# Kernel tuning notes

Measured on AMD Instinct MI355X. Metric: run time of the kernel, lower is better.

## Reference

```python
import jax, jax.numpy as jnp
import numpy as np


def _gcn_conv(x, W, b, src, dst, deg_inv_sqrt, n_nodes):
    # x: [N, Fin], W: [Fin, Fout]; edges (with self-loops): src, dst [E+N]
    h = x @ W  # [N, Fout]
    norm = deg_inv_sqrt[src] * deg_inv_sqrt[dst]  # [E+N]
    msgs = h[src] * norm[:, None]  # gather-multiply
    out = jax.ops.segment_sum(msgs, dst, num_segments=n_nodes)  # scatter-add
    return out + b


def setup_inputs() -> dict:
    key = jax.random.key(0)
    k1, k2, k3, k4 = jax.random.split(key, 4)
    N, E, FIN, HID, OUT = 100000, 3200000, 128, 32, 32
    x = jax.random.normal(k1, (N, FIN), dtype=jnp.float32)
    edge_index = jax.random.randint(k2, (2, E), 0, N, dtype=jnp.int64)
    W1 = jax.random.normal(k3, (FIN, HID), dtype=jnp.float32) * (1.0 / np.sqrt(FIN))
    b1 = jnp.zeros((HID,), dtype=jnp.float32)
    W2 = jax.random.normal(k4, (HID, OUT), dtype=jnp.float32) * (1.0 / np.sqrt(HID))
    b2 = jnp.zeros((OUT,), dtype=jnp.float32)
    return {"x": x, "edge_index": edge_index, "W1": W1, "b1": b1, "W2": W2, "b2": b2}


def reference(x, edge_index, W1, b1, W2, b2):
    n = x.shape[0]
    # GCNConv defaults: add self-loops, symmetric normalization D^-1/2 (A+I) D^-1/2
    loops = jnp.arange(n, dtype=edge_index.dtype)
    src = jnp.concatenate([edge_index[0], loops])
    dst = jnp.concatenate([edge_index[1], loops])
    deg = jax.ops.segment_sum(jnp.ones_like(dst, dtype=x.dtype), dst, num_segments=n)
    deg_inv_sqrt = jnp.where(deg > 0, jax.lax.rsqrt(jnp.maximum(deg, 1.0)), 0.0)
    h = jax.nn.relu(_gcn_conv(x, W1, b1, src, dst, deg_inv_sqrt, n))  # hidden layer + ReLU
    out = jax.nn.relu(_gcn_conv(h, W2, b2, src, dst, deg_inv_sqrt, n))  # last layer + last_activation relu
    return out
```

## Files before the change

kernel.cpp:

```cpp
#include <hip/hip_runtime.h>
#include <hip/hip_fp16.h>

#define FIN 128
#define HID 32
#define BSHIFT 8
#define BNODES 256
#define CHUNK 2048
#define NBMAX 512
#define CAPB 8960
#define G1ROWS 64
#define XPAD 4


__global__ __launch_bounds__(256) void chunk_sort_kernel(const int* __restrict__ src,
                                                         const int* __restrict__ dst,
                                                         int* __restrict__ ec,
                                                         unsigned short* __restrict__ offt,
                                                         int E, int nb) {
    __shared__ int hist[NBMAX];
    __shared__ int pref[NBMAX];
    __shared__ int wsum[128];
    __shared__ int sorted[CHUNK];
    int c = blockIdx.x, t = threadIdx.x;
    int beg = c * CHUNK;
    int cnt = min(CHUNK, E - beg);
    for (int i = t; i < nb; i += 256) hist[i] = 0;
    __syncthreads();
    int bk[8], ent[8];
    #pragma unroll
    for (int j = 0; j < 8; ++j) {
        int i = t + j * 256;
        if (i < cnt) {
            int d = dst[beg + i];
            bk[j]  = ((unsigned)d) >> BSHIFT;
            ent[j] = src[beg + i] | ((d & (BNODES - 1)) << 24);
            atomicAdd(&hist[bk[j]], 1);
        } else bk[j] = -1;
    }
    __syncthreads();
    if (t < 128) {
        int s = 0;
        #pragma unroll
        for (int j = 0; j < 4; ++j) {
            int idx = t * 4 + j;
            int v = (idx < nb) ? hist[idx] : 0;
            pref[idx] = s; s += v;
        }
        wsum[t] = s;
    }
    __syncthreads();
    if (t == 0) { int run = 0; for (int j = 0; j < 128; ++j) { int v = wsum[j]; wsum[j] = run; run += v; } }
    __syncthreads();
    for (int i = t; i < nb; i += 256) { int p = pref[i] + wsum[i >> 2]; pref[i] = p; hist[i] = p; }
    __syncthreads();
    #pragma unroll
    for (int j = 0; j < 8; ++j) {
        if (bk[j] >= 0) {
            int p = atomicAdd(&hist[bk[j]], 1);
            sorted[p] = ent[j];
        }
    }
    __syncthreads();
    for (int i = t; i < cnt; i += 256) ec[(size_t)c * CHUNK + i] = sorted[i];
    unsigned short* row = offt + (size_t)c * (nb + 1);
    for (int i = t; i < nb; i += 256) row[i] = (unsigned short)pref[i];
    if (t == 0) row[nb] = (unsigned short)cnt;
}


__global__ __launch_bounds__(1024) void bucket_build_kernel(const int* __restrict__ ec,
                                                            const unsigned short* __restrict__ offt,
                                                            int* __restrict__ entries,
                                                            float* __restrict__ dinv,
                                                            int* __restrict__ rowbeg,
                                                            int* __restrict__ rowcnt,
                                                            int n, int nb, int nchunks, int cap) {
    __shared__ int raw[CAPB];
    __shared__ int srt[CAPB];
    __shared__ int hist[BNODES];
    __shared__ int pref[BNODES];
    __shared__ int cursor[BNODES];
    __shared__ int wsum[64];
    __shared__ int nfill;
    int b = blockIdx.x, t = threadIdx.x;
    if (t < BNODES) hist[t] = 0;
    if (t == 0) nfill = 0;
    __syncthreads();
    for (int c = t; c < nchunks; c += 1024) {
        const unsigned short* row = offt + (size_t)c * (nb + 1);
        int s = row[b], e2 = row[b + 1];
        int m = e2 - s;
        if (m > 0) {
            int base = atomicAdd(&nfill, m);
            const int* p = ec + (size_t)c * CHUNK + s;
            for (int k = 0; k < m; ++k) {
                int e = p[k];
                if (base + k < CAPB) raw[base + k] = e;
                atomicAdd(&hist[((unsigned)e) >> 24], 1);
            }
        }
    }
    __syncthreads();
    int total = min(nfill, CAPB);
    if (t < 64) {
        int s = 0;
        #pragma unroll
        for (int j = 0; j < 4; ++j) { int v = hist[t * 4 + j]; pref[t * 4 + j] = s; s += v; }
        wsum[t] = s;
    }
    __syncthreads();
    if (t == 0) { int run = 0; for (int j = 0; j < 64; ++j) { int v = wsum[j]; wsum[j] = run; run += v; } }
    __syncthreads();
    if (t < BNODES) { int p = pref[t] + wsum[t >> 2]; pref[t] = p; cursor[t] = p; }
    __syncthreads();
    for (int i = t; i < total; i += 1024) {
        int e = raw[i];
        int p = atomicAdd(&cursor[((unsigned)e) >> 24], 1);
        srt[p] = e;
    }
    __syncthreads();
    int* ep = entries + (size_t)b * cap;
    for (int i = t; i < total; i += 1024) ep[i] = srt[i];
    int node = b * BNODES + t;
    if (t < BNODES && node < n) {
        int deg = hist[t];
        dinv[node]   = rsqrtf((float)deg + 1.0f);
        rowbeg[node] = b * cap + pref[t];
        rowcnt[node] = deg;
    }
}


__global__ __launch_bounds__(256) void gemm1_kernel(const float* __restrict__ x,
                                                    const float* __restrict__ W,
                                                    const float* __restrict__ dinv,
                                                    __half* __restrict__ h16, int n) {
    __shared__ float Ws[FIN * HID];
    __shared__ float xs[G1ROWS][FIN + XPAD];
    int t = threadIdx.x;
    for (int i = t; i < FIN * HID; i += 256) Ws[i] = W[i];
    int row0 = blockIdx.x * G1ROWS;
    for (int idx = t; idx < G1ROWS * (FIN / 4); idx += 256) {
        int r  = idx >> 5;
        int c4 = (idx & 31) * 4;
        int row = row0 + r;
        float4 v = (row < n) ? *(const float4*)&x[(size_t)row * FIN + c4]
                             : make_float4(0.f, 0.f, 0.f, 0.f);
        *(float4*)&xs[r][c4] = v;
    }
    __syncthreads();
    int tr = t >> 3, tc = t & 7;
    int r0 = tr * 2, c0 = tc * 4;
    float4 a0 = make_float4(0.f, 0.f, 0.f, 0.f);
    float4 a1 = make_float4(0.f, 0.f, 0.f, 0.f);
    #pragma unroll 8
    for (int k4 = 0; k4 < FIN / 4; ++k4) {
        float4 xv0 = *(const float4*)&xs[r0][k4 * 4];
        float4 xv1 = *(const float4*)&xs[r0 + 1][k4 * 4];
        float4 w0 = *(const float4*)&Ws[(k4 * 4 + 0) * HID + c0];
        float4 w1 = *(const float4*)&Ws[(k4 * 4 + 1) * HID + c0];
        float4 w2 = *(const float4*)&Ws[(k4 * 4 + 2) * HID + c0];
        float4 w3 = *(const float4*)&Ws[(k4 * 4 + 3) * HID + c0];
        a0.x = fmaf(xv0.x, w0.x, a0.x); a0.y = fmaf(xv0.x, w0.y, a0.y);
        a0.z = fmaf(xv0.x, w0.z, a0.z); a0.w = fmaf(xv0.x, w0.w, a0.w);
        a0.x = fmaf(xv0.y, w1.x, a0.x); a0.y = fmaf(xv0.y, w1.y, a0.y);
        a0.z = fmaf(xv0.y, w1.z, a0.z); a0.w = fmaf(xv0.y, w1.w, a0.w);
        a0.x = fmaf(xv0.z, w2.x, a0.x); a0.y = fmaf(xv0.z, w2.y, a0.y);
        a0.z = fmaf(xv0.z, w2.z, a0.z); a0.w = fmaf(xv0.z, w2.w, a0.w);
        a0.x = fmaf(xv0.w, w3.x, a0.x); a0.y = fmaf(xv0.w, w3.y, a0.y);
        a0.z = fmaf(xv0.w, w3.z, a0.z); a0.w = fmaf(xv0.w, w3.w, a0.w);
        a1.x = fmaf(xv1.x, w0.x, a1.x); a1.y = fmaf(xv1.x, w0.y, a1.y);
        a1.z = fmaf(xv1.x, w0.z, a1.z); a1.w = fmaf(xv1.x, w0.w, a1.w);
        a1.x = fmaf(xv1.y, w1.x, a1.x); a1.y = fmaf(xv1.y, w1.y, a1.y);
        a1.z = fmaf(xv1.y, w1.z, a1.z); a1.w = fmaf(xv1.y, w1.w, a1.w);
        a1.x = fmaf(xv1.z, w2.x, a1.x); a1.y = fmaf(xv1.z, w2.y, a1.y);
        a1.z = fmaf(xv1.z, w2.z, a1.z); a1.w = fmaf(xv1.z, w2.w, a1.w);
        a1.x = fmaf(xv1.w, w3.x, a1.x); a1.y = fmaf(xv1.w, w3.y, a1.y);
        a1.z = fmaf(xv1.w, w3.z, a1.z); a1.w = fmaf(xv1.w, w3.w, a1.w);
    }
    #pragma unroll
    for (int rr = 0; rr < 2; ++rr) {
        int row = row0 + r0 + rr;
        float4 a = rr ? a1 : a0;
        float sc = (row < n) ? dinv[row] : 0.f;
        __half2 p0 = __floats2half2_rn(a.x * sc, a.y * sc);
        __half2 p1 = __floats2half2_rn(a.z * sc, a.w * sc);
        __half2* dst = (__half2*)&h16[(size_t)row * HID + c0];
        dst[0] = p0;
        dst[1] = p1;
    }
}


__global__ __launch_bounds__(256) void gather_kernel(const int* __restrict__ entries,
                                                     const int* __restrict__ rowbeg,
                                                     const int* __restrict__ rowcnt,
                                                     const float* __restrict__ dinv,
                                                     const __half* __restrict__ h16,
                                                     const float* __restrict__ bias,
                                                     float* __restrict__ out, int n, int sent) {
    int t = threadIdx.x;
    int g = t >> 2, q = t & 3;
    int i = blockIdx.x * 64 + g;
    if (i >= n) return;
    float di = dinv[i];
    float s0, s1, s2, s3, s4, s5, s6, s7;
    {
        float4 raw = *(const float4*)&h16[(size_t)i * HID + q * 8];
        __half2 h0 = *(__half2*)&raw.x, h1 = *(__half2*)&raw.y;
        __half2 h2 = *(__half2*)&raw.z, h3 = *(__half2*)&raw.w;
        float2 f0 = __half22float2(h0), f1 = __half22float2(h1);
        float2 f2 = __half22float2(h2), f3 = __half22float2(h3);
        s0 = f0.x; s1 = f0.y; s2 = f1.x; s3 = f1.y;
        s4 = f2.x; s5 = f2.y; s6 = f3.x; s7 = f3.y;
    }
    int beg = rowbeg[i], cnt = rowcnt[i];
    for (int base = 0; base < cnt; base += 4) {
        int e[4];
        #pragma unroll
        for (int u = 0; u < 4; ++u)
            e[u] = (base + u < cnt) ? (entries[beg + base + u] & 0xFFFFFF) : sent;
        float4 raw[4];
        #pragma unroll
        for (int u = 0; u < 4; ++u)
            raw[u] = *(const float4*)&h16[(size_t)e[u] * HID + q * 8];
        #pragma unroll
        for (int u = 0; u < 4; ++u) {
            __half2 h0 = *(__half2*)&raw[u].x, h1 = *(__half2*)&raw[u].y;
            __half2 h2 = *(__half2*)&raw[u].z, h3 = *(__half2*)&raw[u].w;
            float2 f0 = __half22float2(h0), f1 = __half22float2(h1);
            float2 f2 = __half22float2(h2), f3 = __half22float2(h3);
            s0 += f0.x; s1 += f0.y; s2 += f1.x; s3 += f1.y;
            s4 += f2.x; s5 += f2.y; s6 += f3.x; s7 += f3.y;
        }
    }
    float4 b0 = *(const float4*)&bias[q * 8];
    float4 b1 = *(const float4*)&bias[q * 8 + 4];
    float4 o0, o1;
    o0.x = fmaxf(b0.x + di * s0, 0.f); o0.y = fmaxf(b0.y + di * s1, 0.f);
    o0.z = fmaxf(b0.z + di * s2, 0.f); o0.w = fmaxf(b0.w + di * s3, 0.f);
    o1.x = fmaxf(b1.x + di * s4, 0.f); o1.y = fmaxf(b1.y + di * s5, 0.f);
    o1.z = fmaxf(b1.z + di * s6, 0.f); o1.w = fmaxf(b1.w + di * s7, 0.f);
    float* op = &out[(size_t)i * HID + q * 8];
    *(float4*)op = o0;
    *(float4*)(op + 4) = o1;
}


__global__ __launch_bounds__(256) void gemm2_kernel(const float* __restrict__ hin,
                                                    const float* __restrict__ W,
                                                    const float* __restrict__ dinv,
                                                    __half* __restrict__ h16, int n) {
    __shared__ float Ws[HID * HID];
    __shared__ float hs[G1ROWS][HID + XPAD];
    int t = threadIdx.x;
    for (int i = t; i < HID * HID; i += 256) Ws[i] = W[i];
    int row0 = blockIdx.x * G1ROWS;
    for (int idx = t; idx < G1ROWS * (HID / 4); idx += 256) {
        int r  = idx >> 3;
        int c4 = (idx & 7) * 4;
        int row = row0 + r;
        float4 v = (row < n) ? *(const float4*)&hin[(size_t)row * HID + c4]
                             : make_float4(0.f, 0.f, 0.f, 0.f);
        *(float4*)&hs[r][c4] = v;
    }
    __syncthreads();
    int tr = t >> 3, tc = t & 7;
    int r0 = tr * 2, c0 = tc * 4;
    float4 a0 = make_float4(0.f, 0.f, 0.f, 0.f);
    float4 a1 = make_float4(0.f, 0.f, 0.f, 0.f);
    #pragma unroll
    for (int k4 = 0; k4 < HID / 4; ++k4) {
        float4 xv0 = *(const float4*)&hs[r0][k4 * 4];
        float4 xv1 = *(const float4*)&hs[r0 + 1][k4 * 4];
        float4 w0 = *(const float4*)&Ws[(k4 * 4 + 0) * HID + c0];
        float4 w1 = *(const float4*)&Ws[(k4 * 4 + 1) * HID + c0];
        float4 w2 = *(const float4*)&Ws[(k4 * 4 + 2) * HID + c0];
        float4 w3 = *(const float4*)&Ws[(k4 * 4 + 3) * HID + c0];
        a0.x = fmaf(xv0.x, w0.x, a0.x); a0.y = fmaf(xv0.x, w0.y, a0.y);
        a0.z = fmaf(xv0.x, w0.z, a0.z); a0.w = fmaf(xv0.x, w0.w, a0.w);
        a0.x = fmaf(xv0.y, w1.x, a0.x); a0.y = fmaf(xv0.y, w1.y, a0.y);
        a0.z = fmaf(xv0.y, w1.z, a0.z); a0.w = fmaf(xv0.y, w1.w, a0.w);
        a0.x = fmaf(xv0.z, w2.x, a0.x); a0.y = fmaf(xv0.z, w2.y, a0.y);
        a0.z = fmaf(xv0.z, w2.z, a0.z); a0.w = fmaf(xv0.z, w2.w, a0.w);
        a0.x = fmaf(xv0.w, w3.x, a0.x); a0.y = fmaf(xv0.w, w3.y, a0.y);
        a0.z = fmaf(xv0.w, w3.z, a0.z); a0.w = fmaf(xv0.w, w3.w, a0.w);
        a1.x = fmaf(xv1.x, w0.x, a1.x); a1.y = fmaf(xv1.x, w0.y, a1.y);
        a1.z = fmaf(xv1.x, w0.z, a1.z); a1.w = fmaf(xv1.x, w0.w, a1.w);
        a1.x = fmaf(xv1.y, w1.x, a1.x); a1.y = fmaf(xv1.y, w1.y, a1.y);
        a1.z = fmaf(xv1.y, w1.z, a1.z); a1.w = fmaf(xv1.y, w1.w, a1.w);
        a1.x = fmaf(xv1.z, w2.x, a1.x); a1.y = fmaf(xv1.z, w2.y, a1.y);
        a1.z = fmaf(xv1.z, w2.z, a1.z); a1.w = fmaf(xv1.z, w2.w, a1.w);
        a1.x = fmaf(xv1.w, w3.x, a1.x); a1.y = fmaf(xv1.w, w3.y, a1.y);
        a1.z = fmaf(xv1.w, w3.z, a1.z); a1.w = fmaf(xv1.w, w3.w, a1.w);
    }
    #pragma unroll
    for (int rr = 0; rr < 2; ++rr) {
        int row = row0 + r0 + rr;
        float4 a = rr ? a1 : a0;
        float sc = (row < n) ? dinv[row] : 0.f;
        __half2 p0 = __floats2half2_rn(a.x * sc, a.y * sc);
        __half2 p1 = __floats2half2_rn(a.z * sc, a.w * sc);
        __half2* dst = (__half2*)&h16[(size_t)row * HID + c0];
        dst[0] = p0;
        dst[1] = p1;
    }
}

extern "C" void kernel_launch(void* const* d_in, const int* in_sizes, int n_in,
                              void* d_out, int out_size, void* d_ws, size_t ws_size,
                              hipStream_t stream) {
    const float* x  = (const float*)d_in[0];
    const int*   ei = (const int*)d_in[1];
    const float* W1 = (const float*)d_in[2];
    const float* b1 = (const float*)d_in[3];
    const float* W2 = (const float*)d_in[4];
    const float* b2 = (const float*)d_in[5];
    float* out = (float*)d_out;

    int n = in_sizes[0] / FIN;
    int E = in_sizes[1] / 2;
    const int* src = ei;
    const int* dst = ei + E;

    int nb = (n + BNODES - 1) / BNODES;
    int nchunks = (E + CHUNK - 1) / CHUNK;
    int ggrid = (n + G1ROWS) / G1ROWS;
    int npad = ggrid * G1ROWS;
    int cap = CAPB;

    char* ws = (char*)d_ws;
    size_t off = 0;
    auto alloc = [&](size_t bytes) { char* p = ws + off; off += (bytes + 255) & ~(size_t)255; return p; };
    int*            ec      = (int*)alloc((size_t)nchunks * CHUNK * 4);
    unsigned short* offt    = (unsigned short*)alloc((size_t)nchunks * (nb + 1) * 2);
    int*            entries = (int*)alloc((size_t)nb * cap * 4);
    float*          dinv    = (float*)alloc((size_t)n * 4);
    int*            rowbeg  = (int*)alloc((size_t)n * 4);
    int*            rowcnt  = (int*)alloc((size_t)n * 4);
    float*          acc     = (float*)alloc((size_t)n * HID * 4);
    __half*         hh      = (__half*)alloc((size_t)npad * HID * 2);

    chunk_sort_kernel<<<nchunks, 256, 0, stream>>>(src, dst, ec, offt, E, nb);
    bucket_build_kernel<<<nb, 1024, 0, stream>>>(ec, offt, entries, dinv, rowbeg, rowcnt,
                                                 n, nb, nchunks, cap);

    gemm1_kernel<<<ggrid, 256, 0, stream>>>(x, W1, dinv, hh, n);
    gather_kernel<<<(n + 63) / 64, 256, 0, stream>>>(entries, rowbeg, rowcnt, dinv, hh, b1, acc, n, n);

    gemm2_kernel<<<ggrid, 256, 0, stream>>>(acc, W2, dinv, hh, n);
    gather_kernel<<<(n + 63) / 64, 256, 0, stream>>>(entries, rowbeg, rowcnt, dinv, hh, b2, out, n, n);
}
```

Baseline: 292.1 us.

## Remap gather to 16 lanes per node with shuffled edge indices

The gather kernel now assigns 16 threads per destination node, each owning two features (a half2), instead of 4 threads each owning 8 features. Each lane loads one edge index per batch of 16 neighbors, and the lanes share indices through width-16 shuffles, so index loads are coalesced rather than redundantly reloaded by every lane. The intent is more independent row loads in flight and less per-thread index traffic. The cost is 4-byte loads per lane instead of 16-byte loads, extra shuffle instructions, and wasted work on sentinel rows when a node's degree is not a multiple of 16.

Measured after the change: 253.2 us. -13.3%, faster.

```diff
diff --git a/kernel.cpp b/kernel.cpp
--- a/kernel.cpp
+++ b/kernel.cpp
@@ -200,50 +200,41 @@
                                                      const float* __restrict__ bias,
                                                      float* __restrict__ out, int n, int sent) {
     int t = threadIdx.x;
-    int g = t >> 2, q = t & 3;
-    int i = blockIdx.x * 64 + g;
+    int g = t >> 4, f = t & 15;
+    int i = blockIdx.x * 16 + g;
     if (i >= n) return;
     float di = dinv[i];
-    float s0, s1, s2, s3, s4, s5, s6, s7;
+    float s0, s1;
     {
-        float4 raw = *(const float4*)&h16[(size_t)i * HID + q * 8];
-        __half2 h0 = *(__half2*)&raw.x, h1 = *(__half2*)&raw.y;
-        __half2 h2 = *(__half2*)&raw.z, h3 = *(__half2*)&raw.w;
-        float2 f0 = __half22float2(h0), f1 = __half22float2(h1);
-        float2 f2 = __half22float2(h2), f3 = __half22float2(h3);
-        s0 = f0.x; s1 = f0.y; s2 = f1.x; s3 = f1.y;
-        s4 = f2.x; s5 = f2.y; s6 = f3.x; s7 = f3.y;
+        __half2 h = *(const __half2*)&h16[(size_t)i * HID + f * 2];
+        float2 fp = __half22float2(h);
+        s0 = fp.x; s1 = fp.y;
     }
     int beg = rowbeg[i], cnt = rowcnt[i];
-    for (int base = 0; base < cnt; base += 4) {
-        int e[4];
+    for (int base = 0; base < cnt; base += 16) {
+        int idx = beg + base + f;
+        int sv = ((base + f) < cnt) ? entries[idx] : sent;
+        sv &= 0xFFFFFF;
         #pragma unroll
-        for (int u = 0; u < 4; ++u)
-            e[u] = (base + u < cnt) ? (entries[beg + base + u] & 0xFFFFFF) : sent;
-        float4 raw[4];
-        #pragma unroll
-        for (int u = 0; u < 4; ++u)
-            raw[u] = *(const float4*)&h16[(size_t)e[u] * HID + q * 8];
-        #pragma unroll
-        for (int u = 0; u < 4; ++u) {
-            __half2 h0 = *(__half2*)&raw[u].x, h1 = *(__half2*)&raw[u].y;
-            __half2 h2 = *(__half2*)&raw[u].z, h3 = *(__half2*)&raw[u].w;
-            float2 f0 = __half22float2(h0), f1 = __half22float2(h1);
-            float2 f2 = __half22float2(h2), f3 = __half22float2(h3);
-            s0 += f0.x; s1 += f0.y; s2 += f1.x; s3 += f1.y;
-            s4 += f2.x; s5 += f2.y; s6 += f3.x; s7 += f3.y;
+        for (int j0 = 0; j0 < 16; j0 += 8) {
+            __half2 hv[8];
+            #pragma unroll
+            for (int j = 0; j < 8; ++j) {
+                int e = __shfl(sv, j0 + j, 16);
+                hv[j] = *(const __half2*)&h16[(size_t)e * HID + f * 2];
+            }
+            #pragma unroll
+            for (int j = 0; j < 8; ++j) {
+                s0 += __half2float(__low2half(hv[j]));
+                s1 += __half2float(__high2half(hv[j]));
+            }
         }
     }
-    float4 b0 = *(const float4*)&bias[q * 8];
-    float4 b1 = *(const float4*)&bias[q * 8 + 4];
-    float4 o0, o1;
-    o0.x = fmaxf(b0.x + di * s0, 0.f); o0.y = fmaxf(b0.y + di * s1, 0.f);
-    o0.z = fmaxf(b0.z + di * s2, 0.f); o0.w = fmaxf(b0.w + di * s3, 0.f);
-    o1.x = fmaxf(b1.x + di * s4, 0.f); o1.y = fmaxf(b1.y + di * s5, 0.f);
-    o1.z = fmaxf(b1.z + di * s6, 0.f); o1.w = fmaxf(b1.w + di * s7, 0.f);
-    float* op = &out[(size_t)i * HID + q * 8];
-    *(float4*)op = o0;
-    *(float4*)(op + 4) = o1;
+    float2 b2 = *(const float2*)&bias[f * 2];
+    float2 o;
+    o.x = fmaxf(b2.x + di * s0, 0.f);
+    o.y = fmaxf(b2.y + di * s1, 0.f);
+    *(float2*)&out[(size_t)i * HID + f * 2] = o;
 }
 
 
@@ -346,8 +337,8 @@
                                                  n, nb, nchunks, cap);
 
     gemm1_kernel<<<ggrid, 256, 0, stream>>>(x, W1, dinv, hh, n);
-    gather_kernel<<<(n + 63) / 64, 256, 0, stream>>>(entries, rowbeg, rowcnt, dinv, hh, b1, acc, n, n);
+    gather_kernel<<<(n + 15) / 16, 256, 0, stream>>>(entries, rowbeg, rowcnt, dinv, hh, b1, acc, n, n);
 
     gemm2_kernel<<<ggrid, 256, 0, stream>>>(acc, W2, dinv, hh, n);
-    gather_kernel<<<(n + 63) / 64, 256, 0, stream>>>(entries, rowbeg, rowcnt, dinv, hh, b2, out, n, n);
-}
+    gather_kernel<<<(n + 15) / 16, 256, 0, stream>>>(entries, rowbeg, rowcnt, dinv, hh, b2, out, n, n);
+}
```
